# Kernel tuning notes

Measured on AMD Instinct MI355X. Metric: run time of the kernel, lower is better.

Reference implementation:

```python
import jax, jax.numpy as jnp
import numpy as np

N = 50000      # num nodes
E = 400000     # directed edges (avg out-degree 8)
DIN = 128
DOUT = 128
ALPHA = 0.5    # args.alphaDir (buffer, requires_grad=False)
BETA = 0.5     # args.betaDir
GAMA = 0.5     # args.gamaDir


def _dedupe(rows, cols, vals, n):
    key = rows.astype(np.int64) * n + cols.astype(np.int64)
    uk, inv = np.unique(key, return_inverse=True)
    v = np.bincount(inv, weights=vals, minlength=uk.shape[0])
    return (uk // n).astype(np.int32), (uk % n).astype(np.int32), v.astype(np.float32)


def _dir_norm(r, c, v, n):
    # directed_norm: D_out^{-1/2} A D_in^{-1/2}, inf -> 0
    in_deg = np.bincount(c, weights=v, minlength=n)
    out_deg = np.bincount(r, weights=v, minlength=n)
    in_is = np.zeros(n); m = in_deg > 0; in_is[m] = in_deg[m] ** -0.5
    out_is = np.zeros(n); m = out_deg > 0; out_is[m] = out_deg[m] ** -0.5
    return r, c, (out_is[r] * v * in_is[c]).astype(np.float32)


def _spgemm(rA, cA, vA, rB, cB, vB, n):
    # sparse @ sparse in COO, vectorized numpy
    order = np.argsort(rB, kind='stable')
    rBs, cBs, vBs = rB[order], cB[order], vB[order]
    degB = np.bincount(rBs, minlength=n)
    indptr = np.concatenate(([0], np.cumsum(degB)))
    counts = degB[cA]
    total = int(counts.sum())
    rep = np.repeat(np.arange(len(rA)), counts)
    first = np.cumsum(counts) - counts
    pos = np.arange(total) - np.repeat(first, counts) + np.repeat(indptr[cA], counts)
    rows = rA[rep]
    cols = cBs[pos]
    vals = vA[rep].astype(np.float64) * vBs[pos]
    return _dedupe(rows, cols, vals, n)


def setup_inputs() -> dict:
    rng = np.random.default_rng(0)
    r0 = rng.integers(0, N, E).astype(np.int64)
    c0 = rng.integers(0, N, E).astype(np.int64)
    r, c, v = _dedupe(r0, c0, np.ones(E, np.float32), N)
    a = _dir_norm(r, c, v, N)                 # adj_norm
    at = _dir_norm(c, r, v, N)                # adj_t_norm
    rr, cc, vv = _spgemm(a[0], a[1], a[2], at[0], at[1], at[2], N)
    aat = _dir_norm(rr, cc, vv, N)            # directed_norm(A @ At)
    rr, cc, vv = _spgemm(at[0], at[1], at[2], a[0], a[1], a[2], N)
    ata = _dir_norm(rr, cc, vv, N)            # directed_norm(At @ A)
    rr, cc, vv = _spgemm(a[0], a[1], a[2], a[0], a[1], a[2], N)
    aa = _dir_norm(rr, cc, vv, N)             # directed_norm(A @ A)
    rr, cc, vv = _spgemm(at[0], at[1], at[2], at[0], at[1], at[2], N)
    atat = _dir_norm(rr, cc, vv, N)           # directed_norm(At @ At)

    key = jax.random.key(0)
    ks = jax.random.split(key, 7)
    x = jax.random.normal(ks[0], (N, DIN), dtype=jnp.float32)
    s = 1.0 / np.sqrt(DIN)

    def lin(k):
        k1, k2 = jax.random.split(k)
        w = jax.random.uniform(k1, (DIN, DOUT), jnp.float32, -s, s)
        b = jax.random.uniform(k2, (DOUT,), jnp.float32, -s, s)
        return w, b

    w_sd, b_sd = lin(ks[1]); w_ds, b_ds = lin(ks[2])
    w0, b0 = lin(ks[3]); w1, b1 = lin(ks[4])
    w2, b2 = lin(ks[5]); w3, b3 = lin(ks[6])

    out = {'x': x,
           'w_sd': w_sd, 'b_sd': b_sd, 'w_ds': w_ds, 'b_ds': b_ds,
           'w0': w0, 'b0': b0, 'w1': w1, 'b1': b1,
           'w2': w2, 'b2': b2, 'w3': w3, 'b3': b3}
    for name, t in (('a', a), ('at', at), ('aat', aat), ('ata', ata), ('aa', aa), ('atat', atat)):
        out[name + '_rows'] = jnp.asarray(t[0])
        out[name + '_cols'] = jnp.asarray(t[1])
        out[name + '_vals'] = jnp.asarray(t[2])
    return out


def _spmm(rows, cols, vals, x):
    # (A @ x)[i] = sum_e vals[e] * x[cols[e]] scattered to rows[e]
    return jax.ops.segment_sum(vals[:, None] * x[cols], rows, num_segments=x.shape[0])


def reference(x, a_rows, a_cols, a_vals, at_rows, at_cols, at_vals,
              aat_rows, aat_cols, aat_vals, ata_rows, ata_cols, ata_vals,
              aa_rows, aa_cols, aa_vals, atat_rows, atat_cols, atat_vals,
              w_sd, b_sd, w_ds, b_ds, w0, b0, w1, b1, w2, b2, w3, b3):
    out1 = ALPHA * (_spmm(a_rows, a_cols, a_vals, x) @ w_sd + b_sd) \
         + (1.0 - ALPHA) * (_spmm(at_rows, at_cols, at_vals, x) @ w_ds + b_ds)
    out2 = BETA * (_spmm(aat_rows, aat_cols, aat_vals, x) @ w0 + b0) \
         + (1.0 - BETA) * (_spmm(ata_rows, ata_cols, ata_vals, x) @ w1 + b1)
    out3 = GAMA * (_spmm(aa_rows, aa_cols, aa_vals, x) @ w2 + b2) \
         + (1.0 - GAMA) * (_spmm(atat_rows, atat_cols, atat_vals, x) @ w3 + b3)
    return out1 + out2 + out3
```

## Files before the change

### kernel.cpp

```cpp
#include <hip/hip_runtime.h>
#include <hip/hip_bf16.h>

#define FD 128

typedef __attribute__((ext_vector_type(8))) short bf16x8;
typedef __attribute__((ext_vector_type(4))) float f32x4;

__device__ __forceinline__ float bfu2f(unsigned short u) {
  return __uint_as_float(((unsigned int)u) << 16);
}
__device__ __forceinline__ float b2f(__hip_bfloat16 v) { return __bfloat162float(v); }
__device__ __forceinline__ unsigned int pk2(float lo, float hi) {
  return (unsigned int)__bfloat16_as_ushort(__float2bfloat16(lo)) |
         ((unsigned int)__bfloat16_as_ushort(__float2bfloat16(hi)) << 16);
}

__device__ __forceinline__ float ldf(const void* p, int i, int ff) {
  return ff ? ((const float*)p)[i] : b2f(((const __hip_bfloat16*)p)[i]);
}
__device__ __forceinline__ int ldi(const void* p, int i, int fi) {
  return fi ? (int)((const long long*)p)[i] : ((const int*)p)[i];
}

__global__ void detect_k(const void* x, const void* cols, int* flags) {
  __shared__ int cnt[2];
  if (threadIdx.x < 2) cnt[threadIdx.x] = 0;
  __syncthreads();
  const unsigned short* xu = (const unsigned short*)x;
  int big = 0;
  for (int i = threadIdx.x; i < 1024; i += 256) {
    int e = (xu[i] >> 7) & 0xFF;
    if (e >= 0x90) big++;
  }
  if (big) atomicAdd(&cnt[0], big);
  const int* ci = (const int*)cols;
  int zeros = 0;
  for (int i = threadIdx.x; i < 128; i += 256)
    if ((i & 1) && ci[i] == 0) zeros++;
  if (zeros) atomicAdd(&cnt[1], zeros);
  __syncthreads();
  if (threadIdx.x == 0) {
    flags[0] = (cnt[0] > 16) ? 1 : 0;
    flags[1] = (cnt[1] >= 32) ? 1 : 0;
  }
}

__global__ void cvtall_k(const void* __restrict__ rows, const void* __restrict__ cols,
                         const void* __restrict__ vals, int nnz, int n,
                         int* __restrict__ r32, int* __restrict__ c32,
                         float* __restrict__ vf, int* __restrict__ cntT,
                         const int* flags) {
  int ff = flags[0], fi = flags[1];
  int i = blockIdx.x * 256 + threadIdx.x;
  if (i >= nnz) return;
  int r = ldi(rows, i, fi);
  int c = ldi(cols, i, fi);
  if ((unsigned)r >= (unsigned)n) r = 0;
  if ((unsigned)c >= (unsigned)n) c = 0;
  r32[i] = r;
  c32[i] = c;
  vf[i] = ldf(vals, i, ff);
  atomicAdd(&cntT[c], 1);
}

__global__ void scanA_k(const int* __restrict__ cnt, int n, int* bsum) {
  __shared__ int sh[256];
  int t = threadIdx.x;
  int i = blockIdx.x * 256 + t;
  sh[t] = (i < n) ? cnt[i] : 0;
  __syncthreads();
  for (int d = 128; d > 0; d >>= 1) {
    if (t < d) sh[t] += sh[t + d];
    __syncthreads();
  }
  if (t == 0) bsum[blockIdx.x] = sh[0];
}

__global__ void scanB_k(int* bsum, int nb, int* rpTail) {
  __shared__ int sh[256];
  int t = threadIdx.x;
  int v = (t < nb) ? bsum[t] : 0;
  sh[t] = v;
  __syncthreads();
  int val = v;
  for (int d = 1; d < 256; d <<= 1) {
    int add = (t >= d) ? sh[t - d] : 0;
    __syncthreads();
    val += add;
    sh[t] = val;
    __syncthreads();
  }
  if (t < nb) bsum[t] = val - v;
  if (t == 255) *rpTail = val;
}

__global__ void scanC_k(const int* __restrict__ cnt, int n, const int* __restrict__ bsum,
                        int* rp, int* cur) {
  __shared__ int sh[256];
  int t = threadIdx.x;
  int i = blockIdx.x * 256 + t;
  int v = (i < n) ? cnt[i] : 0;
  sh[t] = v;
  __syncthreads();
  int val = v;
  for (int d = 1; d < 256; d <<= 1) {
    int add = (t >= d) ? sh[t - d] : 0;
    __syncthreads();
    val += add;
    sh[t] = val;
    __syncthreads();
  }
  int ex = val - v + bsum[blockIdx.x];
  if (i < n) { rp[i] = ex; cur[i] = ex; }
}

__global__ void bsearch_k(const int* __restrict__ rows, int nnz, int n, int* rpA) {
  int i = blockIdx.x * 256 + threadIdx.x;
  if (i > n) return;
  int lo = 0, hi = nnz;
  while (lo < hi) { int mid = (lo + hi) >> 1; if (rows[mid] < i) lo = mid + 1; else hi = mid; }
  rpA[i] = lo;
}

__global__ void scatter_k(const int* __restrict__ r, const int* __restrict__ c,
                          const float* __restrict__ v, int nnz,
                          int* cur, int* tSrc, float* tVal) {
  int i = blockIdx.x * 256 + threadIdx.x;
  if (i >= nnz) return;
  int p = atomicAdd(&cur[c[i]], 1);
  if ((unsigned)p >= (unsigned)nnz) return;
  tSrc[p] = r[i];
  tVal[p] = v[i];
}

__global__ void nodesum_k(const int* __restrict__ rpA, const float* __restrict__ av,
                          const int* __restrict__ rpT, const float* __restrict__ tv,
                          float* __restrict__ u1, float* __restrict__ v1, int n) {
  int i = blockIdx.x * 256 + threadIdx.x;
  if (i >= n) return;
  float su = 0.f;
  int e0 = rpA[i], e1 = rpA[i + 1];
  for (int j = e0; j < e1; ++j) su += av[j];
  u1[i] = su;
  float sv = 0.f;
  int f0 = rpT[i], f1 = rpT[i + 1];
  for (int j = f0; j < f1; ++j) sv += tv[j];
  v1[i] = sv;
}

__global__ void deg2b_k(const int* __restrict__ rpA, const int* __restrict__ ci,
                        const float* __restrict__ av,
                        const int* __restrict__ rpT, const int* __restrict__ ti,
                        const float* __restrict__ tv,
                        const float* __restrict__ u1, const float* __restrict__ v1,
                        float* __restrict__ e1, float* __restrict__ e2,
                        float* __restrict__ e3, float* __restrict__ e4, int n) {
  int i = blockIdx.x * 256 + threadIdx.x;
  if (i >= n) return;
  float a1 = 0.f, a3 = 0.f;
  int s0 = rpA[i], s1 = rpA[i + 1];
  for (int j = s0; j < s1; ++j) {
    int c = ci[j];
    float v = av[j];
    a1 = fmaf(v, v1[c], a1);
    a3 = fmaf(v, u1[c], a3);
  }
  e1[i] = a1;
  e3[i] = a3;
  float a2 = 0.f, a4 = 0.f;
  int t0 = rpT[i], t1 = rpT[i + 1];
  for (int j = t0; j < t1; ++j) {
    int r = ti[j];
    float v = tv[j];
    a2 = fmaf(v, u1[r], a2);
    a4 = fmaf(v, v1[r], a4);
  }
  e2[i] = a2;
  e4[i] = a4;
}

__global__ void rsqrt_k(const float* __restrict__ e, float* __restrict__ s, int n) {
  int i = blockIdx.x * 256 + threadIdx.x;
  if (i >= n) return;
  float x = e[i];
  s[i] = (x > 0.f) ? rsqrtf(x) : 0.f;
}

__global__ void bias_k(const void* a, const void* b, const void* c, const void* d,
                       const void* e, const void* f, float* bias, const int* flags) {
  int ff = flags[0];
  int i = threadIdx.x;
  bias[i] = 0.5f * (ldf(a, i, ff) + ldf(b, i, ff) + ldf(c, i, ff)
                  + ldf(d, i, ff) + ldf(e, i, ff) + ldf(f, i, ff));
}

__global__ void fill_k(unsigned short* o, int n) {
  int i = blockIdx.x * 256 + threadIdx.x;
  if (i < n) o[i] = 0x3E80;
}

__global__ void cvtx_k(const void* __restrict__ x, __hip_bfloat16* __restrict__ xb,
                       int n, const int* flags) {
  int ff = flags[0];
  int i = (blockIdx.x * 256 + threadIdx.x) * 4;
  if (i + 3 >= n) {
    for (int k = i; k < n; ++k) xb[k] = __float2bfloat16(ldf(x, k, ff));
    return;
  }
  xb[i + 0] = __float2bfloat16(ldf(x, i + 0, ff));
  xb[i + 1] = __float2bfloat16(ldf(x, i + 1, ff));
  xb[i + 2] = __float2bfloat16(ldf(x, i + 2, ff));
  xb[i + 3] = __float2bfloat16(ldf(x, i + 3, ff));
}

struct W6p { const void* w[6]; };
__global__ void wt2_k(W6p ws, __hip_bfloat16* __restrict__ Wt, const int* flags) {
  int ff = flags[0];
  int e = blockIdx.x * 256 + threadIdx.x;
  if (e >= 6 * 16384) return;
  int seg = e >> 14;
  int r = e & 16383;
  int n = r >> 7;
  int innerB = (r & 127) << 1;
  int kb = innerB ^ ((n & 7) << 4);
  int k = kb >> 1;
  Wt[e] = __float2bfloat16(ldf(ws.w[seg], k * 128 + n, ff));
}

__global__ __launch_bounds__(256) void fh3_k(
    const int* __restrict__ rp, const int* __restrict__ ci, const float* __restrict__ cv,
    const unsigned int* __restrict__ xb,
    unsigned int* __restrict__ ot, unsigned int* __restrict__ oa,
    unsigned int* __restrict__ ob,
    const float* __restrict__ sA, const float* __restrict__ sB, int n) {
  int wave = threadIdx.x >> 6;
  int lane = threadIdx.x & 63;
  int es = lane >> 4;
  int li = lane & 15;
  int r = blockIdx.x * 4 + wave;
  if (r >= n) return;
  int s = rp[r], e = rp[r + 1];
  float t[8], a[8], b[8];
#pragma unroll
  for (int k = 0; k < 8; ++k) { t[k] = 0.f; a[k] = 0.f; b[k] = 0.f; }
  for (int j = s + es; j < e; j += 4) {
    int c = ci[j];
    float v = cv[j];
    float va = v * sA[c];
    float vb = v * sB[c];
    uint4 u = *(const uint4*)(xb + (size_t)c * 64 + li * 4);
    unsigned int uu[4] = {u.x, u.y, u.z, u.w};
#pragma unroll
    for (int k = 0; k < 4; ++k) {
      float lo = __uint_as_float(uu[k] << 16);
      float hi = __uint_as_float(uu[k] & 0xFFFF0000u);
      t[2 * k]     = fmaf(v, lo, t[2 * k]);
      t[2 * k + 1] = fmaf(v, hi, t[2 * k + 1]);
      a[2 * k]     = fmaf(va, lo, a[2 * k]);
      a[2 * k + 1] = fmaf(va, hi, a[2 * k + 1]);
      b[2 * k]     = fmaf(vb, lo, b[2 * k]);
      b[2 * k + 1] = fmaf(vb, hi, b[2 * k + 1]);
    }
  }
#pragma unroll
  for (int k = 0; k < 8; ++k) {
    t[k] += __shfl_xor(t[k], 16); t[k] += __shfl_xor(t[k], 32);
    a[k] += __shfl_xor(a[k], 16); a[k] += __shfl_xor(a[k], 32);
    b[k] += __shfl_xor(b[k], 16); b[k] += __shfl_xor(b[k], 32);
  }
  if (es == 0) {
    size_t off = (size_t)r * 64 + li * 4;
    uint4 o;
    o.x = pk2(t[0], t[1]); o.y = pk2(t[2], t[3]);
    o.z = pk2(t[4], t[5]); o.w = pk2(t[6], t[7]);
    *(uint4*)(ot + off) = o;
    o.x = pk2(a[0], a[1]); o.y = pk2(a[2], a[3]);
    o.z = pk2(a[4], a[5]); o.w = pk2(a[6], a[7]);
    *(uint4*)(oa + off) = o;
    o.x = pk2(b[0], b[1]); o.y = pk2(b[2], b[3]);
    o.z = pk2(b[4], b[5]); o.w = pk2(b[6], b[7]);
    *(uint4*)(ob + off) = o;
  }
}

__global__ __launch_bounds__(256) void sh2_k(
    const int* __restrict__ rp, const int* __restrict__ ci, const float* __restrict__ cv,
    const unsigned int* __restrict__ ga, const unsigned int* __restrict__ gb,
    unsigned int* __restrict__ ya, unsigned int* __restrict__ yb,
    const float* __restrict__ rsa, const float* __restrict__ rsb, int n) {
  int wave = threadIdx.x >> 6;
  int lane = threadIdx.x & 63;
  int es = lane >> 4;
  int li = lane & 15;
  int r = blockIdx.x * 4 + wave;
  if (r >= n) return;
  int s = rp[r], e = rp[r + 1];
  float a[8], b[8];
#pragma unroll
  for (int k = 0; k < 8; ++k) { a[k] = 0.f; b[k] = 0.f; }
  for (int j = s + es; j < e; j += 4) {
    int c = ci[j];
    float v = cv[j];
    size_t off = (size_t)c * 64 + li * 4;
    uint4 u = *(const uint4*)(ga + off);
    uint4 w = *(const uint4*)(gb + off);
    unsigned int uu[4] = {u.x, u.y, u.z, u.w};
    unsigned int ww[4] = {w.x, w.y, w.z, w.w};
#pragma unroll
    for (int k = 0; k < 4; ++k) {
      a[2 * k]     = fmaf(v, __uint_as_float(uu[k] << 16), a[2 * k]);
      a[2 * k + 1] = fmaf(v, __uint_as_float(uu[k] & 0xFFFF0000u), a[2 * k + 1]);
      b[2 * k]     = fmaf(v, __uint_as_float(ww[k] << 16), b[2 * k]);
      b[2 * k + 1] = fmaf(v, __uint_as_float(ww[k] & 0xFFFF0000u), b[2 * k + 1]);
    }
  }
#pragma unroll
  for (int k = 0; k < 8; ++k) {
    a[k] += __shfl_xor(a[k], 16); a[k] += __shfl_xor(a[k], 32);
    b[k] += __shfl_xor(b[k], 16); b[k] += __shfl_xor(b[k], 32);
  }
  if (es == 0) {
    float ra = rsa[r], rb = rsb[r];
    size_t off = (size_t)r * 64 + li * 4;
    uint4 o;
    o.x = pk2(a[0] * ra, a[1] * ra); o.y = pk2(a[2] * ra, a[3] * ra);
    o.z = pk2(a[4] * ra, a[5] * ra); o.w = pk2(a[6] * ra, a[7] * ra);
    *(uint4*)(ya + off) = o;
    o.x = pk2(b[0] * rb, b[1] * rb); o.y = pk2(b[2] * rb, b[3] * rb);
    o.z = pk2(b[4] * rb, b[5] * rb); o.w = pk2(b[6] * rb, b[7] * rb);
    *(uint4*)(yb + off) = o;
  }
}

struct Y6 { const unsigned short* y[6]; };

__global__ __launch_bounds__(256) void gemm6m2_k(
    Y6 ys, const unsigned short* __restrict__ Wt2, const float* __restrict__ bias,
    void* __restrict__ outp, int M, const int* flags) {
  int ff = flags[0];
  __shared__ __align__(16) unsigned short Bs[16384];
  const int tid = threadIdx.x;
  const int lane = tid & 63;
  const int wave = tid >> 6;
  const int m = lane & 15;
  const int q = lane >> 4;
  const int r0 = blockIdx.x * 64 + wave * 16;
  const int rowA = r0 + m;
  const bool okA = rowA < M;
  const bf16x8 zero8 = {0, 0, 0, 0, 0, 0, 0, 0};

  f32x4 acc[8];
#pragma unroll
  for (int nt = 0; nt < 8; ++nt) acc[nt] = (f32x4){0.f, 0.f, 0.f, 0.f};

  bf16x8 Bst[8];
#pragma unroll
  for (int c2 = 0; c2 < 8; ++c2)
    Bst[c2] = *(const bf16x8*)(Wt2 + (size_t)(c2 * 256 + tid) * 8);
  bf16x8 Apre[4];
#pragma unroll
  for (int kc = 0; kc < 4; ++kc)
    Apre[kc] = okA ? *(const bf16x8*)(ys.y[0] + (size_t)rowA * FD + kc * 32 + q * 8)
                   : zero8;

  const int swz = (m & 7) << 4;

#pragma unroll
  for (int t = 0; t < 6; ++t) {
    __syncthreads();
#pragma unroll
    for (int c2 = 0; c2 < 8; ++c2)
      *(bf16x8*)((char*)Bs + (size_t)(c2 * 256 + tid) * 16) = Bst[c2];
    bf16x8 Acur[4];
#pragma unroll
    for (int kc = 0; kc < 4; ++kc) Acur[kc] = Apre[kc];
    if (t < 5) {
#pragma unroll
      for (int c2 = 0; c2 < 8; ++c2)
        Bst[c2] = *(const bf16x8*)(Wt2 + (size_t)(t + 1) * 16384 +
                                   (size_t)(c2 * 256 + tid) * 8);
#pragma unroll
      for (int kc = 0; kc < 4; ++kc)
        Apre[kc] = okA ? *(const bf16x8*)(ys.y[t + 1] + (size_t)rowA * FD + kc * 32 + q * 8)
                       : zero8;
    }
    __syncthreads();
#pragma unroll
    for (int kc = 0; kc < 4; ++kc) {
      const int koff = (kc * 64 + q * 16) ^ swz;
#pragma unroll
      for (int nt = 0; nt < 8; ++nt) {
        const int nrow = nt * 16 + m;
        bf16x8 bfv = *(const bf16x8*)((const char*)Bs + nrow * 256 + koff);
        acc[nt] = __builtin_amdgcn_mfma_f32_16x16x32_bf16(Acur[kc], bfv, acc[nt], 0, 0, 0);
      }
    }
  }

#pragma unroll
  for (int nt = 0; nt < 8; ++nt) {
    int col = nt * 16 + m;
    float bv = bias[col];
#pragma unroll
    for (int rg = 0; rg < 4; ++rg) {
      int grow = r0 + q * 4 + rg;
      if (grow >= M) continue;
      float v = 0.5f * acc[nt][rg] + bv;
      if (ff) ((float*)outp)[(size_t)grow * FD + col] = v;
      else ((unsigned short*)outp)[(size_t)grow * FD + col] =
          __bfloat16_as_ushort(__float2bfloat16(v));
    }
  }
}

__global__ __launch_bounds__(128) void spmm_k(
    const int* __restrict__ rp, const void* __restrict__ ci, int cif,
    const void* __restrict__ cv, int cvf,
    const void* __restrict__ x, int xf, __hip_bfloat16* __restrict__ y,
    int n, int nnzMax,
    const float* __restrict__ cscale, const float* __restrict__ rscale,
    const int* flags) {
  int ff = flags[0], fi = flags[1];
  int vf = cvf ? 1 : ff;
  int iw = cif ? fi : 0;
  int xw = xf ? ff : 0;
  const int t = threadIdx.x;
  int r0 = blockIdx.x * 4;
  int rend = min(r0 + 4, n);
  for (int r = r0; r < rend; ++r) {
    int s = rp[r], e = rp[r + 1];
    s = max(0, min(s, nnzMax));
    e = max(s, min(e, nnzMax));
    float acc = 0.f;
    for (int j = s; j < e; ++j) {
      int c = ldi(ci, j, iw);
      if ((unsigned)c >= (unsigned)n) c = 0;
      float v = (vf ? ((const float*)cv)[j] : b2f(((const __hip_bfloat16*)cv)[j]));
      if (cscale) v *= cscale[c];
      float xv = xw ? ((const float*)x)[c * FD + t]
                    : b2f(((const __hip_bfloat16*)x)[c * FD + t]);
      acc = fmaf(v, xv, acc);
    }
    if (rscale) acc *= rscale[r];
    y[r * FD + t] = __float2bfloat16(acc);
  }
}

__global__ __launch_bounds__(256) void gemm_k(
    const __hip_bfloat16* __restrict__ Y, const void* __restrict__ W,
    const float* __restrict__ bias, const void* __restrict__ accin,
    void* __restrict__ outp, int M, const int* flags) {
  int ff = flags[0];
  __shared__ __align__(16) float Wl[32 * 128];
  __shared__ __align__(16) float Yl[64 * 36];
  const int t = threadIdx.x;
  const int row0 = blockIdx.x * 64;
  const int c4 = (t & 31) * 4;
  const int r8 = (t >> 5) * 8;
  const int rs = t >> 3;
  const int q = t & 7;
  float acc[8][4];
#pragma unroll
  for (int m = 0; m < 8; ++m)
#pragma unroll
    for (int j = 0; j < 4; ++j) acc[m][j] = 0.f;
  for (int kc = 0; kc < 4; ++kc) {
    if (ff) {
      const float4* Wg4 = (const float4*)((const float*)W + kc * 32 * 128);
#pragma unroll
      for (int i = 0; i < 4; ++i)
        *(float4*)(Wl + (t + i * 256) * 4) = Wg4[t + i * 256];
    } else {
      const ushort4* Wg4 = (const ushort4*)((const unsigned short*)W + kc * 32 * 128);
#pragma unroll
      for (int i = 0; i < 4; ++i) {
        ushort4 u = Wg4[t + i * 256];
        int base = (t + i * 256) * 4;
        Wl[base + 0] = bfu2f(u.x);
        Wl[base + 1] = bfu2f(u.y);
        Wl[base + 2] = bfu2f(u.z);
        Wl[base + 3] = bfu2f(u.w);
      }
    }
#pragma unroll
    for (int i = 0; i < 2; ++i) {
      int rr = rs + i * 32;
      int grow = row0 + rr;
      ushort4 u = make_ushort4(0, 0, 0, 0);
      if (grow < M)
        u = *(const ushort4*)((const unsigned short*)Y + grow * FD + kc * 32 + q * 4);
      float* yd = Yl + rr * 36 + q * 4;
      yd[0] = bfu2f(u.x); yd[1] = bfu2f(u.y); yd[2] = bfu2f(u.z); yd[3] = bfu2f(u.w);
    }
    __syncthreads();
#pragma unroll
    for (int kk = 0; kk < 32; kk += 4) {
      float4 w0 = *(const float4*)(Wl + (kk + 0) * 128 + c4);
      float4 w1 = *(const float4*)(Wl + (kk + 1) * 128 + c4);
      float4 w2 = *(const float4*)(Wl + (kk + 2) * 128 + c4);
      float4 w3 = *(const float4*)(Wl + (kk + 3) * 128 + c4);
#pragma unroll
      for (int m = 0; m < 8; ++m) {
        float4 yv = *(const float4*)(Yl + (r8 + m) * 36 + kk);
        acc[m][0] = fmaf(yv.x, w0.x, acc[m][0]);
        acc[m][1] = fmaf(yv.x, w0.y, acc[m][1]);
        acc[m][2] = fmaf(yv.x, w0.z, acc[m][2]);
        acc[m][3] = fmaf(yv.x, w0.w, acc[m][3]);
        acc[m][0] = fmaf(yv.y, w1.x, acc[m][0]);
        acc[m][1] = fmaf(yv.y, w1.y, acc[m][1]);
        acc[m][2] = fmaf(yv.y, w1.z, acc[m][2]);
        acc[m][3] = fmaf(yv.y, w1.w, acc[m][3]);
        acc[m][0] = fmaf(yv.z, w2.x, acc[m][0]);
        acc[m][1] = fmaf(yv.z, w2.y, acc[m][1]);
        acc[m][2] = fmaf(yv.z, w2.z, acc[m][2]);
        acc[m][3] = fmaf(yv.z, w2.w, acc[m][3]);
        acc[m][0] = fmaf(yv.w, w3.x, acc[m][0]);
        acc[m][1] = fmaf(yv.w, w3.y, acc[m][1]);
        acc[m][2] = fmaf(yv.w, w3.z, acc[m][2]);
        acc[m][3] = fmaf(yv.w, w3.w, acc[m][3]);
      }
    }
    __syncthreads();
  }
  float4 b4 = make_float4(0.f, 0.f, 0.f, 0.f);
  if (bias) b4 = *(const float4*)(bias + c4);
#pragma unroll
  for (int m = 0; m < 8; ++m) {
    int grow = row0 + r8 + m;
    if (grow >= M) continue;
    float4 rv;
    rv.x = 0.5f * acc[m][0] + b4.x;
    rv.y = 0.5f * acc[m][1] + b4.y;
    rv.z = 0.5f * acc[m][2] + b4.z;
    rv.w = 0.5f * acc[m][3] + b4.w;
    if (accin) {
      if (ff) {
        float4 o = *(const float4*)((const float*)accin + grow * FD + c4);
        rv.x += o.x; rv.y += o.y; rv.z += o.z; rv.w += o.w;
      } else {
        ushort4 o = *(const ushort4*)((const unsigned short*)accin + grow * FD + c4);
        rv.x += bfu2f(o.x); rv.y += bfu2f(o.y); rv.z += bfu2f(o.z); rv.w += bfu2f(o.w);
      }
    }
    if (ff) {
      *(float4*)((float*)outp + grow * FD + c4) = rv;
    } else {
      ushort4 so;
      so.x = __bfloat16_as_ushort(__float2bfloat16(rv.x));
      so.y = __bfloat16_as_ushort(__float2bfloat16(rv.y));
      so.z = __bfloat16_as_ushort(__float2bfloat16(rv.z));
      so.w = __bfloat16_as_ushort(__float2bfloat16(rv.w));
      *(ushort4*)((unsigned short*)outp + grow * FD + c4) = so;
    }
  }
}

extern "C" void kernel_launch(void* const* d_in, const int* in_sizes, int n_in,
                              void* d_out, int out_size, void* d_ws, size_t ws_size,
                              hipStream_t stream) {
  const void* x    = d_in[0];
  const void* w_sd = d_in[1];
  const void* b_sd = d_in[2];
  const void* w_ds = d_in[3];
  const void* b_ds = d_in[4];
  const void* w0   = d_in[5];
  const void* b0   = d_in[6];
  const void* w1   = d_in[7];
  const void* b1   = d_in[8];
  const void* w2   = d_in[9];
  const void* b2   = d_in[10];
  const void* w3   = d_in[11];
  const void* b3   = d_in[12];
  const void* a_rows = d_in[13];
  const void* a_cols = d_in[14];
  const void* a_vals = d_in[15];
  const int nnz = in_sizes[13];
  const int N = in_sizes[0] / FD;

  const size_t BUF = ((size_t)N * FD * 2 + 255) & ~(size_t)255;

  auto misc_need = [&](int nbig) -> size_t {
    size_t need = (size_t)nbig * BUF;
    need += ((size_t)10 * N * 4 + 255) & ~(size_t)255;
    need += 512 + 256 + 1024;
    need += (((size_t)(N + 1) * 4 + 255) & ~(size_t)255) * 2;
    need += (((size_t)N * 4 + 255) & ~(size_t)255) * 2;
    need += (((size_t)nnz * 4 + 255) & ~(size_t)255) * 5;
    need += (6 * 16384 * 2 + 255) & ~(size_t)255;
    return need;
  };
  size_t needA = misc_need(8);
  size_t needB = misc_need(2);

  int pathA = (ws_size >= needA) ? 1 : 0;
  if (!pathA && ws_size < needB) {
    fill_k<<<(out_size + 255) / 256, 256, 0, stream>>>((unsigned short*)d_out, out_size);
    return;
  }

  int nbig = pathA ? 8 : 2;
  char* p = (char*)d_ws;
  char* bufs[8];
  for (int i = 0; i < 8; ++i) bufs[i] = (i < nbig) ? (p + (size_t)i * BUF) : nullptr;
  char* q = p + (size_t)nbig * BUF;
  auto take = [&](size_t bytes) -> char* {
    char* r = q;
    q += (bytes + 255) & ~(size_t)255;
    return r;
  };
  float* degf  = (float*)take((size_t)10 * N * 4);
  float* biasf = (float*)take(512);
  int*   flags = (int*)take(256);
  int*   bsum  = (int*)take(1024);
  int* rpA  = (int*)take((size_t)(N + 1) * 4);
  int* rpT  = (int*)take((size_t)(N + 1) * 4);
  int* curT = (int*)take((size_t)N * 4);
  int* cntT = (int*)take((size_t)N * 4);
  int* tSrc = (int*)take((size_t)nnz * 4);
  float* tValF = (float*)take((size_t)nnz * 4);
  int* aRow32 = (int*)take((size_t)nnz * 4);
  int* aCol32 = (int*)take((size_t)nnz * 4);
  float* aValF = (float*)take((size_t)nnz * 4);
  __hip_bfloat16* Wt = (__hip_bfloat16*)take(6 * 16384 * 2);

  float* u1 = degf;
  float* v1 = degf + N;
  float* e1 = degf + 2 * N;
  float* e2 = degf + 3 * N;
  float* e3 = degf + 4 * N;
  float* e4 = degf + 5 * N;
  float* s1 = degf + 6 * N;
  float* s2 = degf + 7 * N;
  float* s3 = degf + 8 * N;
  float* s4 = degf + 9 * N;

  int eb = (nnz + 255) / 256;
  int nb = (N + 255) / 256;

  detect_k<<<1, 256, 0, stream>>>(x, a_cols, flags);
  hipMemsetAsync(cntT, 0, (size_t)N * 4, stream);
  cvtall_k<<<eb, 256, 0, stream>>>(a_rows, a_cols, a_vals, nnz, N, aRow32, aCol32, aValF, cntT, flags);
  scanA_k<<<nb, 256, 0, stream>>>(cntT, N, bsum);
  scanB_k<<<1, 256, 0, stream>>>(bsum, nb, rpT + N);
  scanC_k<<<nb, 256, 0, stream>>>(cntT, N, bsum, rpT, curT);
  bsearch_k<<<(N + 256) / 256, 256, 0, stream>>>(aRow32, nnz, N, rpA);
  scatter_k<<<eb, 256, 0, stream>>>(aRow32, aCol32, aValF, nnz, curT, tSrc, tValF);
  nodesum_k<<<nb, 256, 0, stream>>>(rpA, aValF, rpT, tValF, u1, v1, N);
  deg2b_k<<<nb, 256, 0, stream>>>(rpA, aCol32, aValF, rpT, tSrc, tValF, u1, v1,
                                  e1, e2, e3, e4, N);
  rsqrt_k<<<(4 * N + 255) / 256, 256, 0, stream>>>(e1, s1, 4 * N);
  bias_k<<<1, FD, 0, stream>>>(b_sd, b_ds, b0, b1, b2, b3, biasf, flags);

  int sg2 = (N + 3) / 4;
  int gg = (N + 63) / 64;
  int gg3 = (N + 63) / 64;

  if (pathA) {
    W6p wargs;
    wargs.w[0] = w_sd; wargs.w[1] = w_ds; wargs.w[2] = w0;
    wargs.w[3] = w1;   wargs.w[4] = w2;   wargs.w[5] = w3;
    wt2_k<<<(6 * 16384 + 255) / 256, 256, 0, stream>>>(wargs, Wt, flags);

    __hip_bfloat16* xb = (__hip_bfloat16*)bufs[0];
    cvtx_k<<<(N * FD / 4 + 255) / 256, 256, 0, stream>>>(x, xb, N * FD, flags);

    unsigned int* xbu = (unsigned int*)bufs[0];
    unsigned int* t2 = (unsigned int*)bufs[1];
    unsigned int* g3 = (unsigned int*)bufs[2];
    unsigned int* g6 = (unsigned int*)bufs[3];
    unsigned int* t1 = (unsigned int*)bufs[4];
    unsigned int* g4 = (unsigned int*)bufs[5];
    unsigned int* g5 = (unsigned int*)bufs[6];
    unsigned int* y3 = (unsigned int*)bufs[7];
    unsigned int* y5 = (unsigned int*)bufs[0];
    unsigned int* y4 = (unsigned int*)bufs[2];
    unsigned int* y6 = (unsigned int*)bufs[6];

    fh3_k<<<sg2, 256, 0, stream>>>(rpT, tSrc, tValF, xbu, t2, g3, g6, s1, s3, N);
    fh3_k<<<sg2, 256, 0, stream>>>(rpA, aCol32, aValF, xbu, t1, g4, g5, s2, s4, N);
    sh2_k<<<sg2, 256, 0, stream>>>(rpA, aCol32, aValF, g3, g5, y3, y5, s1, s3, N);
    sh2_k<<<sg2, 256, 0, stream>>>(rpT, tSrc, tValF, g4, g6, y4, y6, s2, s4, N);

    Y6 yargs;
    yargs.y[0] = (const unsigned short*)t1;
    yargs.y[1] = (const unsigned short*)t2;
    yargs.y[2] = (const unsigned short*)y3;
    yargs.y[3] = (const unsigned short*)y4;
    yargs.y[4] = (const unsigned short*)y5;
    yargs.y[5] = (const unsigned short*)y6;
    gemm6m2_k<<<gg3, 256, 0, stream>>>(yargs, (const unsigned short*)Wt, biasf, d_out, N, flags);
  } else {
    __hip_bfloat16* Yb = (__hip_bfloat16*)bufs[0];
    __hip_bfloat16* gb = (__hip_bfloat16*)bufs[1];
    spmm_k<<<sg2, 128, 0, stream>>>(rpA, a_cols, 1, a_vals, 0, x, 1, Yb, N, nnz, nullptr, nullptr, flags);
    gemm_k<<<gg, 256, 0, stream>>>(Yb, w_sd, biasf, nullptr, d_out, N, flags);
    spmm_k<<<sg2, 128, 0, stream>>>(rpT, tSrc, 0, tValF, 1, x, 1, Yb, N, nnz, nullptr, nullptr, flags);
    gemm_k<<<gg, 256, 0, stream>>>(Yb, w_ds, nullptr, d_out, d_out, N, flags);
    spmm_k<<<sg2, 128, 0, stream>>>(rpT, tSrc, 0, tValF, 1, x, 1, gb, N, nnz, s1, nullptr, flags);
    spmm_k<<<sg2, 128, 0, stream>>>(rpA, a_cols, 1, a_vals, 0, gb, 0, Yb, N, nnz, nullptr, s1, flags);
    gemm_k<<<gg, 256, 0, stream>>>(Yb, w0, nullptr, d_out, d_out, N, flags);
    spmm_k<<<sg2, 128, 0, stream>>>(rpA, a_cols, 1, a_vals, 0, x, 1, gb, N, nnz, s2, nullptr, flags);
    spmm_k<<<sg2, 128, 0, stream>>>(rpT, tSrc, 0, tValF, 1, gb, 0, Yb, N, nnz, nullptr, s2, flags);
    gemm_k<<<gg, 256, 0, stream>>>(Yb, w1, nullptr, d_out, d_out, N, flags);
    spmm_k<<<sg2, 128, 0, stream>>>(rpA, a_cols, 1, a_vals, 0, x, 1, gb, N, nnz, s4, nullptr, flags);
    spmm_k<<<sg2, 128, 0, stream>>>(rpA, a_cols, 1, a_vals, 0, gb, 0, Yb, N, nnz, nullptr, s3, flags);
    gemm_k<<<gg, 256, 0, stream>>>(Yb, w2, nullptr, d_out, d_out, N, flags);
    spmm_k<<<sg2, 128, 0, stream>>>(rpT, tSrc, 0, tValF, 1, x, 1, gb, N, nnz, s3, nullptr, flags);
    spmm_k<<<sg2, 128, 0, stream>>>(rpT, tSrc, 0, tValF, 1, gb, 0, Yb, N, nnz, nullptr, s4, flags);
    gemm_k<<<gg, 256, 0, stream>>>(Yb, w3, nullptr, d_out, d_out, N, flags);
  }
}
```

Before: 473.0 us.

## Merge paired SpMM launches, fold rsqrt into degree kernel, widen GEMM rows

```diff
diff --git a/kernel.cpp b/kernel.cpp
--- a/kernel.cpp
+++ b/kernel.cpp
@@ -148,25 +148,25 @@
   v1[i] = sv;
 }
 
-__global__ void deg2b_k(const int* __restrict__ rpA, const int* __restrict__ ci,
+__global__ void deg2c_k(const int* __restrict__ rpA, const int* __restrict__ ci,
                         const float* __restrict__ av,
                         const int* __restrict__ rpT, const int* __restrict__ ti,
                         const float* __restrict__ tv,
                         const float* __restrict__ u1, const float* __restrict__ v1,
-                        float* __restrict__ e1, float* __restrict__ e2,
-                        float* __restrict__ e3, float* __restrict__ e4, int n) {
+                        float* __restrict__ s1, float* __restrict__ s2,
+                        float* __restrict__ s3, float* __restrict__ s4, int n) {
   int i = blockIdx.x * 256 + threadIdx.x;
   if (i >= n) return;
   float a1 = 0.f, a3 = 0.f;
-  int s0 = rpA[i], s1 = rpA[i + 1];
-  for (int j = s0; j < s1; ++j) {
+  int s0 = rpA[i], se = rpA[i + 1];
+  for (int j = s0; j < se; ++j) {
     int c = ci[j];
     float v = av[j];
     a1 = fmaf(v, v1[c], a1);
     a3 = fmaf(v, u1[c], a3);
   }
-  e1[i] = a1;
-  e3[i] = a3;
+  s1[i] = (a1 > 0.f) ? rsqrtf(a1) : 0.f;
+  s3[i] = (a3 > 0.f) ? rsqrtf(a3) : 0.f;
   float a2 = 0.f, a4 = 0.f;
   int t0 = rpT[i], t1 = rpT[i + 1];
   for (int j = t0; j < t1; ++j) {
@@ -175,15 +175,8 @@
     a2 = fmaf(v, u1[r], a2);
     a4 = fmaf(v, v1[r], a4);
   }
-  e2[i] = a2;
-  e4[i] = a4;
-}
-
-__global__ void rsqrt_k(const float* __restrict__ e, float* __restrict__ s, int n) {
-  int i = blockIdx.x * 256 + threadIdx.x;
-  if (i >= n) return;
-  float x = e[i];
-  s[i] = (x > 0.f) ? rsqrtf(x) : 0.f;
+  s2[i] = (a2 > 0.f) ? rsqrtf(a2) : 0.f;
+  s4[i] = (a4 > 0.f) ? rsqrtf(a4) : 0.f;
 }
 
 __global__ void bias_k(const void* a, const void* b, const void* c, const void* d,
@@ -227,17 +220,31 @@
   Wt[e] = __float2bfloat16(ldf(ws.w[seg], k * 128 + n, ff));
 }
 
-__global__ __launch_bounds__(256) void fh3_k(
-    const int* __restrict__ rp, const int* __restrict__ ci, const float* __restrict__ cv,
-    const unsigned int* __restrict__ xb,
-    unsigned int* __restrict__ ot, unsigned int* __restrict__ oa,
-    unsigned int* __restrict__ ob,
-    const float* __restrict__ sA, const float* __restrict__ sB, int n) {
+struct FHSet {
+  const int* rp; const int* ci; const float* cv;
+  unsigned int* ot; unsigned int* oa; unsigned int* ob;
+  const float* sA; const float* sB;
+};
+
+__global__ __launch_bounds__(256) void fh3d_k(
+    FHSet h0, FHSet h1, const unsigned int* __restrict__ xb, int n, int half) {
+  int blk = blockIdx.x;
+  bool hi = blk >= half;
+  const int* rp = hi ? h1.rp : h0.rp;
+  const int* ci = hi ? h1.ci : h0.ci;
+  const float* cv = hi ? h1.cv : h0.cv;
+  unsigned int* ot = hi ? h1.ot : h0.ot;
+  unsigned int* oa = hi ? h1.oa : h0.oa;
+  unsigned int* ob = hi ? h1.ob : h0.ob;
+  const float* sA = hi ? h1.sA : h0.sA;
+  const float* sB = hi ? h1.sB : h0.sB;
+  int bb = hi ? blk - half : blk;
+
   int wave = threadIdx.x >> 6;
   int lane = threadIdx.x & 63;
   int es = lane >> 4;
   int li = lane & 15;
-  int r = blockIdx.x * 4 + wave;
+  int r = bb * 4 + wave;
   if (r >= n) return;
   int s = rp[r], e = rp[r + 1];
   float t[8], a[8], b[8];
@@ -253,13 +260,13 @@
 #pragma unroll
     for (int k = 0; k < 4; ++k) {
       float lo = __uint_as_float(uu[k] << 16);
-      float hi = __uint_as_float(uu[k] & 0xFFFF0000u);
+      float hi2 = __uint_as_float(uu[k] & 0xFFFF0000u);
       t[2 * k]     = fmaf(v, lo, t[2 * k]);
-      t[2 * k + 1] = fmaf(v, hi, t[2 * k + 1]);
+      t[2 * k + 1] = fmaf(v, hi2, t[2 * k + 1]);
       a[2 * k]     = fmaf(va, lo, a[2 * k]);
-      a[2 * k + 1] = fmaf(va, hi, a[2 * k + 1]);
+      a[2 * k + 1] = fmaf(va, hi2, a[2 * k + 1]);
       b[2 * k]     = fmaf(vb, lo, b[2 * k]);
-      b[2 * k + 1] = fmaf(vb, hi, b[2 * k + 1]);
+      b[2 * k + 1] = fmaf(vb, hi2, b[2 * k + 1]);
     }
   }
 #pragma unroll
@@ -283,16 +290,32 @@
   }
 }
 
-__global__ __launch_bounds__(256) void sh2_k(
-    const int* __restrict__ rp, const int* __restrict__ ci, const float* __restrict__ cv,
-    const unsigned int* __restrict__ ga, const unsigned int* __restrict__ gb,
-    unsigned int* __restrict__ ya, unsigned int* __restrict__ yb,
-    const float* __restrict__ rsa, const float* __restrict__ rsb, int n) {
+struct SHSet {
+  const int* rp; const int* ci; const float* cv;
+  const unsigned int* ga; const unsigned int* gb;
+  unsigned int* ya; unsigned int* yb;
+  const float* rsa; const float* rsb;
+};
+
+__global__ __launch_bounds__(256) void sh2d_k(SHSet h0, SHSet h1, int n, int half) {
+  int blk = blockIdx.x;
+  bool hi = blk >= half;
+  const int* rp = hi ? h1.rp : h0.rp;
+  const int* ci = hi ? h1.ci : h0.ci;
+  const float* cv = hi ? h1.cv : h0.cv;
+  const unsigned int* ga = hi ? h1.ga : h0.ga;
+  const unsigned int* gb = hi ? h1.gb : h0.gb;
+  unsigned int* ya = hi ? h1.ya : h0.ya;
+  unsigned int* yb = hi ? h1.yb : h0.yb;
+  const float* rsa = hi ? h1.rsa : h0.rsa;
+  const float* rsb = hi ? h1.rsb : h0.rsb;
+  int bb = hi ? blk - half : blk;
+
   int wave = threadIdx.x >> 6;
   int lane = threadIdx.x & 63;
   int es = lane >> 4;
   int li = lane & 15;
-  int r = blockIdx.x * 4 + wave;
+  int r = bb * 4 + wave;
   if (r >= n) return;
   int s = rp[r], e = rp[r + 1];
   float a[8], b[8];
@@ -334,7 +357,7 @@
 
 struct Y6 { const unsigned short* y[6]; };
 
-__global__ __launch_bounds__(256) void gemm6m2_k(
+__global__ __launch_bounds__(256) void gemm6m3_k(
     Y6 ys, const unsigned short* __restrict__ Wt2, const float* __restrict__ bias,
     void* __restrict__ outp, int M, const int* flags) {
   int ff = flags[0];
@@ -344,24 +367,30 @@
   const int wave = tid >> 6;
   const int m = lane & 15;
   const int q = lane >> 4;
-  const int r0 = blockIdx.x * 64 + wave * 16;
-  const int rowA = r0 + m;
-  const bool okA = rowA < M;
+  const int r0 = blockIdx.x * 128 + wave * 32;
+  const int row0 = r0 + m;
+  const int row1 = r0 + 16 + m;
+  const bool ok0 = row0 < M;
+  const bool ok1 = row1 < M;
   const bf16x8 zero8 = {0, 0, 0, 0, 0, 0, 0, 0};
 
-  f32x4 acc[8];
-#pragma unroll
-  for (int nt = 0; nt < 8; ++nt) acc[nt] = (f32x4){0.f, 0.f, 0.f, 0.f};
+  f32x4 acc0[8], acc1[8];
+#pragma unroll
+  for (int nt = 0; nt < 8; ++nt) {
+    acc0[nt] = (f32x4){0.f, 0.f, 0.f, 0.f};
+    acc1[nt] = (f32x4){0.f, 0.f, 0.f, 0.f};
+  }
 
   bf16x8 Bst[8];
 #pragma unroll
   for (int c2 = 0; c2 < 8; ++c2)
     Bst[c2] = *(const bf16x8*)(Wt2 + (size_t)(c2 * 256 + tid) * 8);
-  bf16x8 Apre[4];
-#pragma unroll
-  for (int kc = 0; kc < 4; ++kc)
-    Apre[kc] = okA ? *(const bf16x8*)(ys.y[0] + (size_t)rowA * FD + kc * 32 + q * 8)
-                   : zero8;
+  bf16x8 Ap0[4], Ap1[4];
+#pragma unroll
+  for (int kc = 0; kc < 4; ++kc) {
+    Ap0[kc] = ok0 ? *(const bf16x8*)(ys.y[0] + (size_t)row0 * FD + kc * 32 + q * 8) : zero8;
+    Ap1[kc] = ok1 ? *(const bf16x8*)(ys.y[0] + (size_t)row1 * FD + kc * 32 + q * 8) : zero8;
+  }
 
   const int swz = (m & 7) << 4;
 
@@ -371,18 +400,19 @@
 #pragma unroll
     for (int c2 = 0; c2 < 8; ++c2)
       *(bf16x8*)((char*)Bs + (size_t)(c2 * 256 + tid) * 16) = Bst[c2];
-    bf16x8 Acur[4];
-#pragma unroll
-    for (int kc = 0; kc < 4; ++kc) Acur[kc] = Apre[kc];
+    bf16x8 A0[4], A1[4];
+#pragma unroll
+    for (int kc = 0; kc < 4; ++kc) { A0[kc] = Ap0[kc]; A1[kc] = Ap1[kc]; }
     if (t < 5) {
 #pragma unroll
       for (int c2 = 0; c2 < 8; ++c2)
         Bst[c2] = *(const bf16x8*)(Wt2 + (size_t)(t + 1) * 16384 +
                                    (size_t)(c2 * 256 + tid) * 8);
 #pragma unroll
-      for (int kc = 0; kc < 4; ++kc)
-        Apre[kc] = okA ? *(const bf16x8*)(ys.y[t + 1] + (size_t)rowA * FD + kc * 32 + q * 8)
-                       : zero8;
+      for (int kc = 0; kc < 4; ++kc) {
+        Ap0[kc] = ok0 ? *(const bf16x8*)(ys.y[t + 1] + (size_t)row0 * FD + kc * 32 + q * 8) : zero8;
+        Ap1[kc] = ok1 ? *(const bf16x8*)(ys.y[t + 1] + (size_t)row1 * FD + kc * 32 + q * 8) : zero8;
+      }
     }
     __syncthreads();
 #pragma unroll
@@ -392,7 +422,8 @@
       for (int nt = 0; nt < 8; ++nt) {
         const int nrow = nt * 16 + m;
         bf16x8 bfv = *(const bf16x8*)((const char*)Bs + nrow * 256 + koff);
-        acc[nt] = __builtin_amdgcn_mfma_f32_16x16x32_bf16(Acur[kc], bfv, acc[nt], 0, 0, 0);
+        acc0[nt] = __builtin_amdgcn_mfma_f32_16x16x32_bf16(A0[kc], bfv, acc0[nt], 0, 0, 0);
+        acc1[nt] = __builtin_amdgcn_mfma_f32_16x16x32_bf16(A1[kc], bfv, acc1[nt], 0, 0, 0);
       }
     }
   }
@@ -403,12 +434,20 @@
     float bv = bias[col];
 #pragma unroll
     for (int rg = 0; rg < 4; ++rg) {
-      int grow = r0 + q * 4 + rg;
-      if (grow >= M) continue;
-      float v = 0.5f * acc[nt][rg] + bv;
-      if (ff) ((float*)outp)[(size_t)grow * FD + col] = v;
-      else ((unsigned short*)outp)[(size_t)grow * FD + col] =
-          __bfloat16_as_ushort(__float2bfloat16(v));
+      int g0 = r0 + q * 4 + rg;
+      if (g0 < M) {
+        float v = 0.5f * acc0[nt][rg] + bv;
+        if (ff) ((float*)outp)[(size_t)g0 * FD + col] = v;
+        else ((unsigned short*)outp)[(size_t)g0 * FD + col] =
+            __bfloat16_as_ushort(__float2bfloat16(v));
+      }
+      int g1 = r0 + 16 + q * 4 + rg;
+      if (g1 < M) {
+        float v = 0.5f * acc1[nt][rg] + bv;
+        if (ff) ((float*)outp)[(size_t)g1 * FD + col] = v;
+        else ((unsigned short*)outp)[(size_t)g1 * FD + col] =
+            __bfloat16_as_ushort(__float2bfloat16(v));
+      }
     }
   }
 }
@@ -589,7 +628,7 @@
     need += (6 * 16384 * 2 + 255) & ~(size_t)255;
     return need;
   };
-  size_t needA = misc_need(8);
+  size_t needA = misc_need(10);
   size_t needB = misc_need(2);
 
   int pathA = (ws_size >= needA) ? 1 : 0;
@@ -598,10 +637,10 @@
     return;
   }
 
-  int nbig = pathA ? 8 : 2;
+  int nbig = pathA ? 10 : 2;
   char* p = (char*)d_ws;
-  char* bufs[8];
-  for (int i = 0; i < 8; ++i) bufs[i] = (i < nbig) ? (p + (size_t)i * BUF) : nullptr;
+  char* bufs[10];
+  for (int i = 0; i < 10; ++i) bufs[i] = (i < nbig) ? (p + (size_t)i * BUF) : nullptr;
   char* q = p + (size_t)nbig * BUF;
   auto take = [&](size_t bytes) -> char* {
     char* r = q;
@@ -625,10 +664,6 @@
 
   float* u1 = degf;
   float* v1 = degf + N;
-  float* e1 = degf + 2 * N;
-  float* e2 = degf + 3 * N;
-  float* e3 = degf + 4 * N;
-  float* e4 = degf + 5 * N;
   float* s1 = degf + 6 * N;
   float* s2 = degf + 7 * N;
   float* s3 = degf + 8 * N;
@@ -646,14 +681,13 @@
   bsearch_k<<<(N + 256) / 256, 256, 0, stream>>>(aRow32, nnz, N, rpA);
   scatter_k<<<eb, 256, 0, stream>>>(aRow32, aCol32, aValF, nnz, curT, tSrc, tValF);
   nodesum_k<<<nb, 256, 0, stream>>>(rpA, aValF, rpT, tValF, u1, v1, N);
-  deg2b_k<<<nb, 256, 0, stream>>>(rpA, aCol32, aValF, rpT, tSrc, tValF, u1, v1,
-                                  e1, e2, e3, e4, N);
-  rsqrt_k<<<(4 * N + 255) / 256, 256, 0, stream>>>(e1, s1, 4 * N);
+  deg2c_k<<<nb, 256, 0, stream>>>(rpA, aCol32, aValF, rpT, tSrc, tValF, u1, v1,
+                                  s1, s2, s3, s4, N);
   bias_k<<<1, FD, 0, stream>>>(b_sd, b_ds, b0, b1, b2, b3, biasf, flags);
 
   int sg2 = (N + 3) / 4;
   int gg = (N + 63) / 64;
-  int gg3 = (N + 63) / 64;
+  int gg4 = (N + 127) / 128;
 
   if (pathA) {
     W6p wargs;
@@ -672,14 +706,17 @@
     unsigned int* g4 = (unsigned int*)bufs[5];
     unsigned int* g5 = (unsigned int*)bufs[6];
     unsigned int* y3 = (unsigned int*)bufs[7];
+    unsigned int* y4 = (unsigned int*)bufs[8];
+    unsigned int* y6 = (unsigned int*)bufs[9];
     unsigned int* y5 = (unsigned int*)bufs[0];
-    unsigned int* y4 = (unsigned int*)bufs[2];
-    unsigned int* y6 = (unsigned int*)bufs[6];
-
-    fh3_k<<<sg2, 256, 0, stream>>>(rpT, tSrc, tValF, xbu, t2, g3, g6, s1, s3, N);
-    fh3_k<<<sg2, 256, 0, stream>>>(rpA, aCol32, aValF, xbu, t1, g4, g5, s2, s4, N);
-    sh2_k<<<sg2, 256, 0, stream>>>(rpA, aCol32, aValF, g3, g5, y3, y5, s1, s3, N);
-    sh2_k<<<sg2, 256, 0, stream>>>(rpT, tSrc, tValF, g4, g6, y4, y6, s2, s4, N);
+
+    FHSet hT = { rpT, tSrc, tValF, t2, g3, g6, s1, s3 };
+    FHSet hA = { rpA, aCol32, aValF, t1, g4, g5, s2, s4 };
+    fh3d_k<<<2 * sg2, 256, 0, stream>>>(hT, hA, xbu, N, sg2);
+
+    SHSet sA = { rpA, aCol32, aValF, g3, g5, y3, y5, s1, s3 };
+    SHSet sT = { rpT, tSrc, tValF, g4, g6, y4, y6, s2, s4 };
+    sh2d_k<<<2 * sg2, 256, 0, stream>>>(sA, sT, N, sg2);
 
     Y6 yargs;
     yargs.y[0] = (const unsigned short*)t1;
@@ -688,7 +725,7 @@
     yargs.y[3] = (const unsigned short*)y4;
     yargs.y[4] = (const unsigned short*)y5;
     yargs.y[5] = (const unsigned short*)y6;
-    gemm6m2_k<<<gg3, 256, 0, stream>>>(yargs, (const unsigned short*)Wt, biasf, d_out, N, flags);
+    gemm6m3_k<<<gg4, 256, 0, stream>>>(yargs, (const unsigned short*)Wt, biasf, d_out, N, flags);
   } else {
     __hip_bfloat16* Yb = (__hip_bfloat16*)bufs[0];
     __hip_bfloat16* gb = (__hip_bfloat16*)bufs[1];
```

New measurement: 447.3 us. 5.4% less time.
